# Kernel optimization log

Hardware: AMD Instinct MI355X
Metric: run time of the kernel (lower is better)

Reference implementation:

```python
import jax, jax.numpy as jnp
import numpy as np

N, A, C, H, W = 2, 9, 80, 100, 152
STRIDE = 8
IM_H, IM_W = float(H * STRIDE), float(W * STRIDE)
PRE_NMS_THRESH = 0.05
PRE_NMS_TOP_N = 1000
NMS_THRESH = 0.5
POST_TOP_N = 100
MIN_SIZE = 0.0
WX = WY = 10.0
WW = WH = 5.0
BBOX_XFORM_CLIP = float(np.log(1000.0 / 16.0))
CLS_OFFSET = 4096.0  # > max image coord, makes per-class NMS equivalent


def _make_anchors():
    # 3 scales x 3 ratios, base size 32 at stride 8 (FPN P3)
    sizes = 32.0 * np.array([1.0, 2.0 ** (1.0 / 3.0), 2.0 ** (2.0 / 3.0)])
    ratios = np.array([0.5, 1.0, 2.0])
    ws, hs = [], []
    for s in sizes:
        for r in ratios:
            ws.append(s * np.sqrt(1.0 / r))
            hs.append(s * np.sqrt(r))
    ws = np.array(ws)  # [A]
    hs = np.array(hs)
    sx = (np.arange(W) + 0.5) * STRIDE
    sy = (np.arange(H) + 0.5) * STRIDE
    cx, cy = np.meshgrid(sx, sy)  # [H, W]
    cx = cx.reshape(-1, 1)
    cy = cy.reshape(-1, 1)
    x1 = cx - 0.5 * ws
    y1 = cy - 0.5 * hs
    x2 = cx + 0.5 * ws
    y2 = cy + 0.5 * hs
    # layout matches permute_and_flatten: index = (h*W + w)*A + a
    return np.stack([x1, y1, x2, y2], -1).reshape(-1, 4).astype(np.float32)


def setup_inputs() -> dict:
    key = jax.random.key(0)
    k1, k2 = jax.random.split(key)
    # shift logits down so sigmoid scores are mostly below pre_nms_thresh (realistic sparsity)
    box_cls = jax.random.normal(k1, (N, A * C, H, W), dtype=jnp.float32) * 2.0 - 4.0
    box_regression = jax.random.normal(k2, (N, A * 4, H, W), dtype=jnp.float32)
    anchors = jnp.asarray(_make_anchors())  # [H*W*A, 4]
    return {"box_cls": box_cls, "box_regression": box_regression, "anchors": anchors}


def _decode(rel, anc):
    # BoxCoder(weights=(10,10,5,5)).decode, TO_REMOVE = 1
    widths = anc[..., 2] - anc[..., 0] + 1.0
    heights = anc[..., 3] - anc[..., 1] + 1.0
    ctr_x = anc[..., 0] + 0.5 * widths
    ctr_y = anc[..., 1] + 0.5 * heights
    dx = rel[..., 0] / WX
    dy = rel[..., 1] / WY
    dw = jnp.minimum(rel[..., 2] / WW, BBOX_XFORM_CLIP)
    dh = jnp.minimum(rel[..., 3] / WH, BBOX_XFORM_CLIP)
    pcx = dx * widths + ctr_x
    pcy = dy * heights + ctr_y
    pw = jnp.exp(dw) * widths
    ph = jnp.exp(dh) * heights
    return jnp.stack(
        [pcx - 0.5 * pw, pcy - 0.5 * ph, pcx + 0.5 * pw - 1.0, pcy + 0.5 * ph - 1.0], -1)


def _nms_keep(boxes, scores, valid):
    # greedy NMS over boxes already sorted by score desc; returns bool keep [K]
    x1, y1, x2, y2 = boxes[:, 0], boxes[:, 1], boxes[:, 2], boxes[:, 3]
    areas = (x2 - x1 + 1.0) * (y2 - y1 + 1.0)
    iw = jnp.maximum(jnp.minimum(x2[:, None], x2[None, :]) - jnp.maximum(x1[:, None], x1[None, :]) + 1.0, 0.0)
    ih = jnp.maximum(jnp.minimum(y2[:, None], y2[None, :]) - jnp.maximum(y1[:, None], y1[None, :]) + 1.0, 0.0)
    inter = iw * ih
    iou = inter / (areas[:, None] + areas[None, :] - inter)  # [K, K]
    K = boxes.shape[0]

    def step(supp, i):
        ki = valid[i] & jnp.logical_not(supp[i])
        supp = supp | jnp.where(ki, iou[i] > NMS_THRESH, False)
        return supp, ki

    _, keep = jax.lax.scan(step, jnp.zeros(K, dtype=bool), jnp.arange(K))
    return keep


def reference(box_cls, box_regression, anchors):
    n = box_cls.shape[0]
    # permute_and_flatten: [N, A*C, H, W] -> [N, H*W*A, C], then sigmoid
    scores = jax.nn.sigmoid(
        box_cls.reshape(n, A, C, H, W).transpose(0, 3, 4, 1, 2).reshape(n, H * W * A, C))
    regs = box_regression.reshape(n, A, 4, H, W).transpose(0, 3, 4, 1, 2).reshape(n, H * W * A, 4)
    # threshold + capped top-k over flattened (anchor, class) pairs
    masked = jnp.where(scores > PRE_NMS_THRESH, scores, -1.0).reshape(n, -1)
    top_scores, top_idx = jax.lax.top_k(masked, PRE_NMS_TOP_N)  # sorted desc
    loc = top_idx // C            # anchor location
    labels = top_idx % C + 1      # per_class += 1
    valid = top_scores > 0.0      # padded slots have score -1
    reg_sel = jnp.take_along_axis(regs, loc[..., None], axis=1)  # [N, K, 4]
    anc_sel = anchors[loc]                                       # [N, K, 4]
    boxes = _decode(reg_sel, anc_sel)
    # clip_to_image
    x1 = jnp.clip(boxes[..., 0], 0.0, IM_W - 1.0)
    y1 = jnp.clip(boxes[..., 1], 0.0, IM_H - 1.0)
    x2 = jnp.clip(boxes[..., 2], 0.0, IM_W - 1.0)
    y2 = jnp.clip(boxes[..., 3], 0.0, IM_H - 1.0)
    boxes = jnp.stack([x1, y1, x2, y2], -1)
    # remove_small_boxes (TO_REMOVE = 1)
    valid = valid & (x2 - x1 + 1.0 >= MIN_SIZE) & (y2 - y1 + 1.0 >= MIN_SIZE)
    # per-class NMS via class-offset trick (boxes of different classes never overlap)
    off = labels.astype(boxes.dtype)[..., None] * CLS_OFFSET
    keep = jax.vmap(_nms_keep)(boxes + off, top_scores, valid)
    kept_scores = jnp.where(keep & valid, top_scores, -1.0)
    # select_over_all_levels: keep top fpn_post_nms_top_n by score
    final_scores, fidx = jax.lax.top_k(kept_scores, POST_TOP_N)
    final_boxes = jnp.take_along_axis(boxes, fidx[..., None], axis=1)
    final_labels = jnp.where(final_scores > 0.0, jnp.take_along_axis(labels, fidx, axis=1), 0)
    return final_boxes, final_scores, final_labels
```

## Files before the change

### kernel.cpp

```cpp
#include <hip/hip_runtime.h>


#define W_    152
#define H_    100
#define A_    9
#define C_    80
#define HW_   (H_*W_)
#define PER_IMG  (A_*C_*HW_)
#define PER_IMG4 (PER_IMG/4)
#define NBIN  2048
#define BIGB_CAP 24576
#define BIGA_CAP 4096
#define SORTN 2048
#define FASTN 1024
#define NDEC  256
#define THRB 2.0f
#define THRA 3.65f
#define CLIPV 4.135166556742356f

#define TPB      256
#define F4_BATCH 16
#define NBATCH   2
#define CHUNK    (TPB*F4_BATCH*NBATCH)
#define NB_SCAN  ((PER_IMG4 + CHUNK - 1) / CHUNK)
#define LCAPB 256
#define LCAPA 64

#define OFF_CNTA 0
#define OFF_CNTB 8
#define OFF_DEC  256
#define OFF_BIGA (256 + 24576)
#define OFF_BIGB (256 + 24576 + 65536)

typedef unsigned long long u64;

__global__ __launch_bounds__(TPB) void scan_kernel(
    const float* __restrict__ cls,
    unsigned int* __restrict__ cntA,
    unsigned int* __restrict__ cntB,
    u64* __restrict__ bigA,
    float2* __restrict__ bigB) {
  const int n = blockIdx.y;
  const float4* __restrict__ in = reinterpret_cast<const float4*>(cls) + (size_t)n * PER_IMG4;
  __shared__ unsigned int lcntA, lcntB, lbaseA, lbaseB;
  __shared__ u64          lkA[LCAPA];
  __shared__ float        lxB[LCAPB]; __shared__ unsigned int liB[LCAPB];
  if (threadIdx.x == 0) { lcntA = 0; lcntB = 0; }
  __syncthreads();

#pragma unroll
  for (int half = 0; half < NBATCH; ++half) {
    const int hbase = blockIdx.x * CHUNK + half * (TPB * F4_BATCH) + threadIdx.x;
    float4 v[F4_BATCH];
#pragma unroll
    for (int j = 0; j < F4_BATCH; ++j) {
      const int t = hbase + j * TPB;
      v[j] = (t < PER_IMG4) ? in[t]
                            : make_float4(-100.f, -100.f, -100.f, -100.f);
    }
#pragma unroll
    for (int j = 0; j < F4_BATCH; ++j) {
      const float4 vv = v[j];
      const float mx = fmaxf(fmaxf(vv.x, vv.y), fmaxf(vv.z, vv.w));
      if (mx > THRB) {
        const int f0  = (hbase + j * TPB) * 4;
        const int ac  = f0 / HW_;
        const int rem = f0 - ac * HW_;
        const int h   = rem / W_;
        const int w0  = rem - h * W_;
        const int a   = ac / C_;
        const int c   = ac - a * C_;
        const int idx0 = ((h * W_ + w0) * A_ + a) * C_ + c;
        const float xs[4] = {vv.x, vv.y, vv.z, vv.w};
#pragma unroll
        for (int e = 0; e < 4; ++e) {
          const float x = xs[e];
          if (x > THRB) {
            const unsigned idx = (unsigned)(idx0 + e * 720);
            unsigned pos = atomicAdd(&lcntB, 1u);
            if (pos < LCAPB) { lxB[pos] = x; liB[pos] = idx; }
            if (x > THRA) {
              float s = 1.0f / (1.0f + expf(-x));
              unsigned pa = atomicAdd(&lcntA, 1u);
              if (pa < LCAPA)
                lkA[pa] = ((u64)__float_as_uint(s) << 32) |
                          (u64)(0xFFFFFFFFu - idx);
            }
          }
        }
      }
    }
  }
  __syncthreads();
  if (threadIdx.x == 0) {
    unsigned cA = lcntA; if (cA > LCAPA) cA = LCAPA;
    unsigned cB = lcntB; if (cB > LCAPB) cB = LCAPB;
    lbaseA = cA ? atomicAdd(&cntA[n], cA) : 0u;
    lbaseB = cB ? atomicAdd(&cntB[n], cB) : 0u;
    lcntA = cA; lcntB = cB;
  }
  __syncthreads();
  const unsigned cA = lcntA, cB = lcntB;
  if (threadIdx.x < cA) {
    unsigned pos = lbaseA + threadIdx.x;
    if (pos < BIGA_CAP)
      bigA[(size_t)n * BIGA_CAP + pos] = lkA[threadIdx.x];
  }
  for (unsigned e = threadIdx.x; e < cB; e += TPB) {
    unsigned pos = lbaseB + e;
    if (pos < BIGB_CAP)
      bigB[(size_t)n * BIGB_CAP + pos] = make_float2(lxB[e], __uint_as_float(liB[e]));
  }
}

__device__ __forceinline__ void decode_box(
    int idx, float sc, int n,
    const float* __restrict__ reg, const float* __restrict__ anchors,
    float4& o0, float4& o1, float4& o2) {
  int c   = idx % C_;
  int loc = idx / C_;
  int a   = loc % A_;
  int hw  = loc / A_;
  int hh  = hw / W_;
  int ww  = hw - hh * W_;
  int rb  = ((n * A_ + a) * 4) * HW_ + hh * W_ + ww;
  float r0 = reg[rb], r1 = reg[rb + HW_], r2 = reg[rb + 2*HW_], r3 = reg[rb + 3*HW_];
  float4 an = reinterpret_cast<const float4*>(anchors)[loc];
  float wdt = an.z - an.x + 1.0f, hgt = an.w - an.y + 1.0f;
  float cx  = an.x + 0.5f * wdt, cy = an.y + 0.5f * hgt;
  float dx = r0 / 10.0f, dy = r1 / 10.0f;
  float dw = fminf(r2 / 5.0f, CLIPV), dh = fminf(r3 / 5.0f, CLIPV);
  float pcx = dx * wdt + cx, pcy = dy * hgt + cy;
  float pw = expf(dw) * wdt, ph = expf(dh) * hgt;
  float x1 = pcx - 0.5f * pw, y1 = pcy - 0.5f * ph;
  float x2 = pcx + 0.5f * pw - 1.0f, y2 = pcy + 0.5f * ph - 1.0f;
  x1 = fminf(fmaxf(x1, 0.0f), (float)(W_*8) - 1.0f);
  y1 = fminf(fmaxf(y1, 0.0f), (float)(H_*8) - 1.0f);
  x2 = fminf(fmaxf(x2, 0.0f), (float)(W_*8) - 1.0f);
  y2 = fminf(fmaxf(y2, 0.0f), (float)(H_*8) - 1.0f);
  bool valid = sc > 0.0f;
  if ((x2 - x1 + 1.0f < 0.0f) || (y2 - y1 + 1.0f < 0.0f)) valid = false;
  int   label = c + 1;
  float off = (float)label * 4096.0f;
  float ox1 = x1 + off, oy1 = y1 + off, ox2 = x2 + off, oy2 = y2 + off;
  o0 = make_float4(ox1, oy1, ox2, oy2);
  o1 = make_float4(x1, y1, x2, y2);
  o2 = make_float4((ox2 - ox1 + 1.0f) * (oy2 - oy1 + 1.0f),
                   valid ? sc : -1.0f, (float)label, 0.0f);
}

__global__ __launch_bounds__(256) void rank_kernel(
    const unsigned int* __restrict__ cntA,
    const u64* __restrict__ bigA,
    const float* __restrict__ reg, const float* __restrict__ anchors,
    float4* __restrict__ dec) {
  const int n = blockIdx.x >> 5;
  const int b = blockIdx.x & 31;
  const int tid = threadIdx.x;
  __shared__ u64 skl[FASTN];

  int ca = (int)cntA[n]; if (ca > FASTN) ca = FASTN;
#pragma unroll
  for (int r = 0; r < 4; ++r) {
    int j = tid + r * 256;
    skl[j] = (j < ca) ? bigA[(size_t)n * BIGA_CAP + j] : 0ull;
  }
  __syncthreads();

  const int kidx = b * 32 + (tid >> 3);
  const int sub  = tid & 7;
  const u64 ki = skl[kidx];
  int rank = 0;
#pragma unroll 8
  for (int it = 0; it < 128; ++it) {
    int j = sub + it * 8;
    u64 kj = skl[j];
    rank += (int)((kj > ki) | ((kj == ki) & (j < kidx)));
  }
  rank += __shfl_xor(rank, 1);
  rank += __shfl_xor(rank, 2);
  rank += __shfl_xor(rank, 4);
  if (sub == 0 && rank < NDEC && ki != 0ull) {
    int idx = (int)(0xFFFFFFFFu - (unsigned)(ki & 0xFFFFFFFFu));
    float sc = __uint_as_float((unsigned)(ki >> 32));
    float4 o0, o1, o2;
    decode_box(idx, sc, n, reg, anchors, o0, o1, o2);
    float4* d = dec + (size_t)n * (3 * NDEC);
    d[rank]            = o0;
    d[NDEC + rank]     = o1;
    d[2 * NDEC + rank] = o2;
  }
}

__global__ __launch_bounds__(256) void finish_kernel(
    const unsigned int* __restrict__ cntA,
    const unsigned int* __restrict__ cntB,
    const float4* __restrict__ dec,
    const float2* __restrict__ bigB,
    const float* __restrict__ reg, const float* __restrict__ anchors,
    float* __restrict__ out) {
  const int n = blockIdx.x;
  const int tid = threadIdx.x;
  const int lane = tid & 63;

  __shared__ float4 dall[3 * NDEC];
  __shared__ u64 skey[SORTN];
  __shared__ unsigned int shist[NBIN];
  __shared__ unsigned int csum[256];
  __shared__ int s_fb, s_k, s_cut, s_cnt;
  __shared__ float4 fb0[1000], fb1[1000], fb2[1000];
  __shared__ int keptidx[100];
  __shared__ unsigned char skeep[1000];
  float4* d0 = dall;
  float4* d1 = dall + NDEC;
  float4* d2 = dall + 2 * NDEC;

  if (tid == 0) { s_cnt = 0; }
  const int caRaw = (int)cntA[n];
  if (tid == 0) s_fb = (caRaw > FASTN || caRaw < NDEC) ? 1 : 0;

  if (caRaw >= NDEC && caRaw <= FASTN) {
#pragma unroll
    for (int r = 0; r < 3; ++r)
      dall[tid + r * 256] = dec[(size_t)n * (3 * NDEC) + tid + r * 256];
  }
  __syncthreads();

  if (s_fb == 0) {
    if (tid < 64) {
      float ka_x1 = 0, ka_y1 = 0, ka_x2 = 0, ka_y2 = 0, ka_ar = 0;
      float kb_x1 = 0, kb_y1 = 0, kb_x2 = 0, kb_y2 = 0, kb_ar = 0;
      int k = 0;
      for (int i = 0; i < NDEC; ++i) {
        if (k >= 100) break;
        float4 bx = d0[i];
        float4 ai = d2[i];
        float x1 = bx.x, y1 = bx.y, x2 = bx.z, y2 = bx.w, ar = ai.x, sc = ai.y;
        bool sup = false;
        if (lane < k) {
          float iw = fminf(x2, ka_x2) - fmaxf(x1, ka_x1) + 1.0f;
          float ih = fminf(y2, ka_y2) - fmaxf(y1, ka_y1) + 1.0f;
          if (iw > 0.0f && ih > 0.0f) {
            float inter = iw * ih;
            sup = inter / (ar + ka_ar - inter) > 0.5f;
          }
        }
        if (lane + 64 < k) {
          float iw = fminf(x2, kb_x2) - fmaxf(x1, kb_x1) + 1.0f;
          float ih = fminf(y2, kb_y2) - fmaxf(y1, kb_y1) + 1.0f;
          if (iw > 0.0f && ih > 0.0f) {
            float inter = iw * ih;
            sup = sup || (inter / (ar + kb_ar - inter) > 0.5f);
          }
        }
        bool any = __any(sup);
        if ((sc > 0.0f) && !any) {
          if (lane == k)      { ka_x1 = x1; ka_y1 = y1; ka_x2 = x2; ka_y2 = y2; ka_ar = ar; }
          if (lane == k - 64) { kb_x1 = x1; kb_y1 = y1; kb_x2 = x2; kb_y2 = y2; kb_ar = ar; }
          if (lane == 0) keptidx[k] = i;
          ++k;
        }
      }
      if (lane == 0) {
        s_k = k;
        if (k < 100) s_fb = 1;
      }
    }
    __syncthreads();

    if (s_fb == 0) {
      if (tid < 100) {
        int f = keptidx[tid];
        float4 b = d1[f];
        float4 ai = d2[f];
        int ob = (n * 100 + tid) * 4;
        out[ob + 0] = b.x; out[ob + 1] = b.y; out[ob + 2] = b.z; out[ob + 3] = b.w;
        out[800  + n * 100 + tid] = ai.y;
        out[1000 + n * 100 + tid] = ai.z;
      }
      return;
    }
  }
  __syncthreads();

  for (int i = tid; i < NBIN; i += 256) shist[i] = 0;
  __syncthreads();
  int bigc = (int)cntB[n]; if (bigc > BIGB_CAP) bigc = BIGB_CAP;
  const float2* __restrict__ bn = bigB + (size_t)n * BIGB_CAP;
  for (int e = tid; e < bigc; e += 256) {
    float x = bn[e].x;
    int b = (int)((x - THRB) * 256.0f); if (b > NBIN - 1) b = NBIN - 1;
    atomicAdd(&shist[b], 1u);
  }
  __syncthreads();
  {
    unsigned int s = 0;
    for (int b = tid * 8; b < tid * 8 + 8; ++b) s += shist[b];
    csum[tid] = s;
  }
  __syncthreads();
  if (tid == 0) {
    int acc = 0, cut = 0;
    for (int cch = 255; cch >= 0; --cch) {
      int nacc = acc + (int)csum[cch];
      if (nacc >= 1000) {
        int a = acc;
        for (int b = cch * 8 + 7; b >= cch * 8; --b) { a += (int)shist[b]; if (a >= 1000) { cut = b; break; } }
        break;
      }
      acc = nacc;
    }
    s_cut = cut;
  }
  __syncthreads();
  const int cut = s_cut;
  for (int e = tid; e < bigc; e += 256) {
    float2 v = bn[e];
    float x = v.x;
    int b = (int)((x - THRB) * 256.0f); if (b > NBIN - 1) b = NBIN - 1;
    if (b >= cut) {
      float s = 1.0f / (1.0f + expf(-x));
      int pos = atomicAdd(&s_cnt, 1);
      if (pos < SORTN)
        skey[pos] = ((u64)__float_as_uint(s) << 32) |
                    (u64)(0xFFFFFFFFu - __float_as_uint(v.y));
    }
  }
  __syncthreads();
  int cnt = s_cnt; if (cnt > SORTN) cnt = SORTN;
  for (int p = tid; p < SORTN; p += 256)
    if (p >= cnt) skey[p] = 0ull;
  __syncthreads();
  for (int k = 2; k <= SORTN; k <<= 1) {
    for (int j = k >> 1; j > 0; j >>= 1) {
#pragma unroll
      for (int u = 0; u < 8; ++u) {
        int tt = tid + u * 256;
        int ixj = tt ^ j;
        if (ixj > tt) {
          u64 va = skey[tt], vb = skey[ixj];
          bool asc = ((tt & k) == 0);
          if (asc ? (va > vb) : (va < vb)) { skey[tt] = vb; skey[ixj] = va; }
        }
      }
      __syncthreads();
    }
  }
  for (int i = tid; i < 1000; i += 256) {
    u64 key = skey[SORTN - 1 - i];
    bool ok = (i < cnt) && (key != 0ull);
    int   idx = ok ? (int)(0xFFFFFFFFu - (unsigned)(key & 0xFFFFFFFFu)) : 0;
    float sc  = ok ? __uint_as_float((unsigned)(key >> 32)) : -1.0f;
    float4 o0, o1, o2;
    decode_box(idx, sc, n, reg, anchors, o0, o1, o2);
    fb0[i] = o0; fb1[i] = o1; fb2[i] = o2;
  }
  __syncthreads();
  if (tid < 64) {
    float ka_x1 = 0, ka_y1 = 0, ka_x2 = 0, ka_y2 = 0, ka_ar = 0;
    float kb_x1 = 0, kb_y1 = 0, kb_x2 = 0, kb_y2 = 0, kb_ar = 0;
    int k = 0;
    for (int i = 0; i < 1000; ++i) {
      if (k >= 100) break;
      float4 bx = fb0[i];
      float4 ai = fb2[i];
      float x1 = bx.x, y1 = bx.y, x2 = bx.z, y2 = bx.w, ar = ai.x, sc = ai.y;
      bool sup = false;
      if (lane < k) {
        float iw = fminf(x2, ka_x2) - fmaxf(x1, ka_x1) + 1.0f;
        float ih = fminf(y2, ka_y2) - fmaxf(y1, ka_y1) + 1.0f;
        if (iw > 0.0f && ih > 0.0f) {
          float inter = iw * ih;
          sup = inter / (ar + ka_ar - inter) > 0.5f;
        }
      }
      if (lane + 64 < k) {
        float iw = fminf(x2, kb_x2) - fmaxf(x1, kb_x1) + 1.0f;
        float ih = fminf(y2, kb_y2) - fmaxf(y1, kb_y1) + 1.0f;
        if (iw > 0.0f && ih > 0.0f) {
          float inter = iw * ih;
          sup = sup || (inter / (ar + kb_ar - inter) > 0.5f);
        }
      }
      bool any = __any(sup);
      bool valid = sc > 0.0f;
      if (valid && !any) {
        if (lane == k)      { ka_x1 = x1; ka_y1 = y1; ka_x2 = x2; ka_y2 = y2; ka_ar = ar; }
        if (lane == k - 64) { kb_x1 = x1; kb_y1 = y1; kb_x2 = x2; kb_y2 = y2; kb_ar = ar; }
        if (lane == 0) { keptidx[k] = i; skeep[i] = 1; }
        ++k;
      } else if (lane == 0) {
        skeep[i] = 0;
      }
    }
    if (lane == 0) {
      if (k < 100) {
        int fill = k;
        for (int q = 0; q < 1000 && fill < 100; ++q)
          if (!skeep[q]) keptidx[fill++] = q;
      }
      s_k = k;
    }
  }
  __syncthreads();
  if (tid < 100) {
    int f = keptidx[tid];
    bool isk = tid < s_k;
    float4 b = fb1[f];
    float sc  = isk ? fb2[f].y : -1.0f;
    float lab = (sc > 0.0f) ? fb2[f].z : 0.0f;
    int ob = (n * 100 + tid) * 4;
    out[ob + 0] = b.x; out[ob + 1] = b.y; out[ob + 2] = b.z; out[ob + 3] = b.w;
    out[800  + n * 100 + tid] = sc;
    out[1000 + n * 100 + tid] = lab;
  }
}

extern "C" void kernel_launch(void* const* d_in, const int* in_sizes, int n_in,
                              void* d_out, int out_size, void* d_ws, size_t ws_size,
                              hipStream_t stream) {
  const float* cls = (const float*)d_in[0];
  const float* reg = (const float*)d_in[1];
  const float* anc = (const float*)d_in[2];
  float* out = (float*)d_out;
  char* ws = (char*)d_ws;
  unsigned int* cntA = (unsigned int*)(ws + OFF_CNTA);
  unsigned int* cntB = (unsigned int*)(ws + OFF_CNTB);
  float4* dec        = (float4*)(ws + OFF_DEC);
  u64*    bigA       = (u64*)(ws + OFF_BIGA);
  float2* bigB       = (float2*)(ws + OFF_BIGB);

  hipMemsetAsync(d_ws, 0, 16, stream);
  dim3 g1(NB_SCAN, 2);
  scan_kernel<<<g1, TPB, 0, stream>>>(cls, cntA, cntB, bigA, bigB);
  rank_kernel<<<64, 256, 0, stream>>>(cntA, bigA, reg, anc, dec);
  finish_kernel<<<2, 256, 0, stream>>>(cntA, cntB, dec, bigB, reg, anc, out);
}
```

Before: 70.05 us.

## Fuse rank and finish kernels via last-block counter; drop tier-B candidate buffer

Merges the rank and finish kernels into one launch. The last block per image, detected with an atomic done counter and threadfences, performs the NMS finish. The scan kernel no longer collects the lower-threshold candidate list, which removes its shared atomics and global writes. The fallback path instead rescans the full class tensor from a single block, so that rare path becomes far more expensive. The fused kernel also uses much more shared memory, which can lower occupancy for the rank phase.

```diff
diff --git a/kernel.cpp b/kernel.cpp
--- a/kernel.cpp
+++ b/kernel.cpp
@@ -9,7 +9,6 @@
 #define PER_IMG  (A_*C_*HW_)
 #define PER_IMG4 (PER_IMG/4)
 #define NBIN  2048
-#define BIGB_CAP 24576
 #define BIGA_CAP 4096
 #define SORTN 2048
 #define FASTN 1024
@@ -23,29 +22,24 @@
 #define NBATCH   2
 #define CHUNK    (TPB*F4_BATCH*NBATCH)
 #define NB_SCAN  ((PER_IMG4 + CHUNK - 1) / CHUNK)
-#define LCAPB 256
 #define LCAPA 64
 
 #define OFF_CNTA 0
-#define OFF_CNTB 8
+#define OFF_DONE 8
 #define OFF_DEC  256
 #define OFF_BIGA (256 + 24576)
-#define OFF_BIGB (256 + 24576 + 65536)
 
 typedef unsigned long long u64;
 
 __global__ __launch_bounds__(TPB) void scan_kernel(
     const float* __restrict__ cls,
     unsigned int* __restrict__ cntA,
-    unsigned int* __restrict__ cntB,
-    u64* __restrict__ bigA,
-    float2* __restrict__ bigB) {
+    u64* __restrict__ bigA) {
   const int n = blockIdx.y;
   const float4* __restrict__ in = reinterpret_cast<const float4*>(cls) + (size_t)n * PER_IMG4;
-  __shared__ unsigned int lcntA, lcntB, lbaseA, lbaseB;
-  __shared__ u64          lkA[LCAPA];
-  __shared__ float        lxB[LCAPB]; __shared__ unsigned int liB[LCAPB];
-  if (threadIdx.x == 0) { lcntA = 0; lcntB = 0; }
+  __shared__ unsigned int lcntA, lbaseA;
+  __shared__ u64 lkA[LCAPA];
+  if (threadIdx.x == 0) lcntA = 0;
   __syncthreads();
 
 #pragma unroll
@@ -62,7 +56,7 @@
     for (int j = 0; j < F4_BATCH; ++j) {
       const float4 vv = v[j];
       const float mx = fmaxf(fmaxf(vv.x, vv.y), fmaxf(vv.z, vv.w));
-      if (mx > THRB) {
+      if (mx > THRA) {
         const int f0  = (hbase + j * TPB) * 4;
         const int ac  = f0 / HW_;
         const int rem = f0 - ac * HW_;
@@ -75,17 +69,12 @@
 #pragma unroll
         for (int e = 0; e < 4; ++e) {
           const float x = xs[e];
-          if (x > THRB) {
-            const unsigned idx = (unsigned)(idx0 + e * 720);
-            unsigned pos = atomicAdd(&lcntB, 1u);
-            if (pos < LCAPB) { lxB[pos] = x; liB[pos] = idx; }
-            if (x > THRA) {
-              float s = 1.0f / (1.0f + expf(-x));
-              unsigned pa = atomicAdd(&lcntA, 1u);
-              if (pa < LCAPA)
-                lkA[pa] = ((u64)__float_as_uint(s) << 32) |
-                          (u64)(0xFFFFFFFFu - idx);
-            }
+          if (x > THRA) {
+            float s = 1.0f / (1.0f + expf(-x));
+            unsigned pa = atomicAdd(&lcntA, 1u);
+            if (pa < LCAPA)
+              lkA[pa] = ((u64)__float_as_uint(s) << 32) |
+                        (u64)(0xFFFFFFFFu - (unsigned)(idx0 + e * 720));
           }
         }
       }
@@ -94,22 +83,14 @@
   __syncthreads();
   if (threadIdx.x == 0) {
     unsigned cA = lcntA; if (cA > LCAPA) cA = LCAPA;
-    unsigned cB = lcntB; if (cB > LCAPB) cB = LCAPB;
     lbaseA = cA ? atomicAdd(&cntA[n], cA) : 0u;
-    lbaseB = cB ? atomicAdd(&cntB[n], cB) : 0u;
-    lcntA = cA; lcntB = cB;
-  }
-  __syncthreads();
-  const unsigned cA = lcntA, cB = lcntB;
-  if (threadIdx.x < cA) {
+    lcntA = cA;
+  }
+  __syncthreads();
+  if (threadIdx.x < lcntA) {
     unsigned pos = lbaseA + threadIdx.x;
     if (pos < BIGA_CAP)
       bigA[(size_t)n * BIGA_CAP + pos] = lkA[threadIdx.x];
-  }
-  for (unsigned e = threadIdx.x; e < cB; e += TPB) {
-    unsigned pos = lbaseB + e;
-    if (pos < BIGB_CAP)
-      bigB[(size_t)n * BIGB_CAP + pos] = make_float2(lxB[e], __uint_as_float(liB[e]));
   }
 }
 
@@ -149,17 +130,33 @@
                    valid ? sc : -1.0f, (float)label, 0.0f);
 }
 
-__global__ __launch_bounds__(256) void rank_kernel(
+__global__ __launch_bounds__(256) void rank_nms_kernel(
+    const float* __restrict__ cls,
     const unsigned int* __restrict__ cntA,
     const u64* __restrict__ bigA,
     const float* __restrict__ reg, const float* __restrict__ anchors,
-    float4* __restrict__ dec) {
+    unsigned int* __restrict__ done,
+    float4* __restrict__ dec,
+    float* __restrict__ out) {
   const int n = blockIdx.x >> 5;
   const int b = blockIdx.x & 31;
   const int tid = threadIdx.x;
+  const int lane = tid & 63;
+
   __shared__ u64 skl[FASTN];
-
-  int ca = (int)cntA[n]; if (ca > FASTN) ca = FASTN;
+  __shared__ int s_last;
+  __shared__ float4 dall[3 * NDEC];
+  __shared__ int s_fb, s_k, s_cut, s_cnt;
+  __shared__ int keptidx[100];
+  __shared__ u64 skey[SORTN];
+  __shared__ unsigned int shist[NBIN];
+  __shared__ unsigned int csum[256];
+  __shared__ float4 fb0[1000], fb1[1000], fb2[1000];
+  __shared__ unsigned char skeep[1000];
+
+  const int caRaw = (int)cntA[n];
+  int ca = caRaw; if (ca > FASTN) ca = FASTN;
+
 #pragma unroll
   for (int r = 0; r < 4; ++r) {
     int j = tid + r * 256;
@@ -190,41 +187,28 @@
     d[NDEC + rank]     = o1;
     d[2 * NDEC + rank] = o2;
   }
-}
-
-__global__ __launch_bounds__(256) void finish_kernel(
-    const unsigned int* __restrict__ cntA,
-    const unsigned int* __restrict__ cntB,
-    const float4* __restrict__ dec,
-    const float2* __restrict__ bigB,
-    const float* __restrict__ reg, const float* __restrict__ anchors,
-    float* __restrict__ out) {
-  const int n = blockIdx.x;
-  const int tid = threadIdx.x;
-  const int lane = tid & 63;
-
-  __shared__ float4 dall[3 * NDEC];
-  __shared__ u64 skey[SORTN];
-  __shared__ unsigned int shist[NBIN];
-  __shared__ unsigned int csum[256];
-  __shared__ int s_fb, s_k, s_cut, s_cnt;
-  __shared__ float4 fb0[1000], fb1[1000], fb2[1000];
-  __shared__ int keptidx[100];
-  __shared__ unsigned char skeep[1000];
+
+  __threadfence();
+  if (tid == 0) {
+    unsigned old = atomicAdd(&done[n], 1u);
+    s_last = (old == 31u) ? 1 : 0;
+  }
+  __syncthreads();
+  if (!s_last) return;
+  __threadfence();
+
+  if (tid == 0) { s_cnt = 0; s_fb = (caRaw > FASTN || caRaw < NDEC) ? 1 : 0; }
+
+  if (caRaw >= NDEC && caRaw <= FASTN) {
+#pragma unroll
+    for (int r = 0; r < 3; ++r)
+      dall[tid + r * 256] = dec[(size_t)n * (3 * NDEC) + tid + r * 256];
+  }
+  __syncthreads();
+
   float4* d0 = dall;
   float4* d1 = dall + NDEC;
   float4* d2 = dall + 2 * NDEC;
-
-  if (tid == 0) { s_cnt = 0; }
-  const int caRaw = (int)cntA[n];
-  if (tid == 0) s_fb = (caRaw > FASTN || caRaw < NDEC) ? 1 : 0;
-
-  if (caRaw >= NDEC && caRaw <= FASTN) {
-#pragma unroll
-    for (int r = 0; r < 3; ++r)
-      dall[tid + r * 256] = dec[(size_t)n * (3 * NDEC) + tid + r * 256];
-  }
-  __syncthreads();
 
   if (s_fb == 0) {
     if (tid < 64) {
@@ -271,10 +255,10 @@
     if (s_fb == 0) {
       if (tid < 100) {
         int f = keptidx[tid];
-        float4 b = d1[f];
+        float4 bb = d1[f];
         float4 ai = d2[f];
         int ob = (n * 100 + tid) * 4;
-        out[ob + 0] = b.x; out[ob + 1] = b.y; out[ob + 2] = b.z; out[ob + 3] = b.w;
+        out[ob + 0] = bb.x; out[ob + 1] = bb.y; out[ob + 2] = bb.z; out[ob + 3] = bb.w;
         out[800  + n * 100 + tid] = ai.y;
         out[1000 + n * 100 + tid] = ai.z;
       }
@@ -285,17 +269,18 @@
 
   for (int i = tid; i < NBIN; i += 256) shist[i] = 0;
   __syncthreads();
-  int bigc = (int)cntB[n]; if (bigc > BIGB_CAP) bigc = BIGB_CAP;
-  const float2* __restrict__ bn = bigB + (size_t)n * BIGB_CAP;
-  for (int e = tid; e < bigc; e += 256) {
-    float x = bn[e].x;
-    int b = (int)((x - THRB) * 256.0f); if (b > NBIN - 1) b = NBIN - 1;
-    atomicAdd(&shist[b], 1u);
+  const float* __restrict__ cn = cls + (size_t)n * PER_IMG;
+  for (int e = tid; e < PER_IMG; e += 256) {
+    float x = cn[e];
+    if (x > THRB) {
+      int bb = (int)((x - THRB) * 256.0f); if (bb > NBIN - 1) bb = NBIN - 1;
+      atomicAdd(&shist[bb], 1u);
+    }
   }
   __syncthreads();
   {
     unsigned int s = 0;
-    for (int b = tid * 8; b < tid * 8 + 8; ++b) s += shist[b];
+    for (int bb = tid * 8; bb < tid * 8 + 8; ++bb) s += shist[bb];
     csum[tid] = s;
   }
   __syncthreads();
@@ -304,8 +289,8 @@
     for (int cch = 255; cch >= 0; --cch) {
       int nacc = acc + (int)csum[cch];
       if (nacc >= 1000) {
-        int a = acc;
-        for (int b = cch * 8 + 7; b >= cch * 8; --b) { a += (int)shist[b]; if (a >= 1000) { cut = b; break; } }
+        int aa = acc;
+        for (int bb = cch * 8 + 7; bb >= cch * 8; --bb) { aa += (int)shist[bb]; if (aa >= 1000) { cut = bb; break; } }
         break;
       }
       acc = nacc;
@@ -314,16 +299,24 @@
   }
   __syncthreads();
   const int cut = s_cut;
-  for (int e = tid; e < bigc; e += 256) {
-    float2 v = bn[e];
-    float x = v.x;
-    int b = (int)((x - THRB) * 256.0f); if (b > NBIN - 1) b = NBIN - 1;
-    if (b >= cut) {
-      float s = 1.0f / (1.0f + expf(-x));
-      int pos = atomicAdd(&s_cnt, 1);
-      if (pos < SORTN)
-        skey[pos] = ((u64)__float_as_uint(s) << 32) |
-                    (u64)(0xFFFFFFFFu - __float_as_uint(v.y));
+  for (int e = tid; e < PER_IMG; e += 256) {
+    float x = cn[e];
+    if (x > THRB) {
+      int bb = (int)((x - THRB) * 256.0f); if (bb > NBIN - 1) bb = NBIN - 1;
+      if (bb >= cut) {
+        int ac2 = e / HW_;
+        int rem = e - ac2 * HW_;
+        int hh  = rem / W_;
+        int ww  = rem - hh * W_;
+        int a2  = ac2 / C_;
+        int c2  = ac2 - a2 * C_;
+        int jidx = ((hh * W_ + ww) * A_ + a2) * C_ + c2;
+        float s = 1.0f / (1.0f + expf(-x));
+        int pos = atomicAdd(&s_cnt, 1);
+        if (pos < SORTN)
+          skey[pos] = ((u64)__float_as_uint(s) << 32) |
+                      (u64)(0xFFFFFFFFu - (unsigned)jidx);
+      }
     }
   }
   __syncthreads();
@@ -406,11 +399,11 @@
   if (tid < 100) {
     int f = keptidx[tid];
     bool isk = tid < s_k;
-    float4 b = fb1[f];
+    float4 bb = fb1[f];
     float sc  = isk ? fb2[f].y : -1.0f;
     float lab = (sc > 0.0f) ? fb2[f].z : 0.0f;
     int ob = (n * 100 + tid) * 4;
-    out[ob + 0] = b.x; out[ob + 1] = b.y; out[ob + 2] = b.z; out[ob + 3] = b.w;
+    out[ob + 0] = bb.x; out[ob + 1] = bb.y; out[ob + 2] = bb.z; out[ob + 3] = bb.w;
     out[800  + n * 100 + tid] = sc;
     out[1000 + n * 100 + tid] = lab;
   }
@@ -425,14 +418,12 @@
   float* out = (float*)d_out;
   char* ws = (char*)d_ws;
   unsigned int* cntA = (unsigned int*)(ws + OFF_CNTA);
-  unsigned int* cntB = (unsigned int*)(ws + OFF_CNTB);
+  unsigned int* done = (unsigned int*)(ws + OFF_DONE);
   float4* dec        = (float4*)(ws + OFF_DEC);
   u64*    bigA       = (u64*)(ws + OFF_BIGA);
-  float2* bigB       = (float2*)(ws + OFF_BIGB);
 
   hipMemsetAsync(d_ws, 0, 16, stream);
   dim3 g1(NB_SCAN, 2);
-  scan_kernel<<<g1, TPB, 0, stream>>>(cls, cntA, cntB, bigA, bigB);
-  rank_kernel<<<64, 256, 0, stream>>>(cntA, bigA, reg, anc, dec);
-  finish_kernel<<<2, 256, 0, stream>>>(cntA, cntB, dec, bigB, reg, anc, out);
+  scan_kernel<<<g1, TPB, 0, stream>>>(cls, cntA, bigA);
+  rank_nms_kernel<<<64, 256, 0, stream>>>(cls, cntA, bigA, reg, anc, done, dec, out);
 }
```

Result: faster. 65.85 us, median of 2 (-6.0%).
